# Kernel optimization log

Hardware: AMD Instinct MI355X
Metric: run time of the kernel (lower is better)

## Reference

```python
import jax, jax.numpy as jnp
import numpy as np

H = 12          # nheads
SIM_EPS = 1e-8  # SimMatrix eps
LN_EPS = 1e-5   # nn.LayerNorm default eps
SLOPE = 0.01    # LeakyReLU default negative slope


def leaky(x):
    return jnp.where(x >= 0, x, SLOPE * x)


def etc_attention(hiddens, gamma, beta, Wout, bout):
    # hiddens: [B, L, 3*D]
    B, L, D3 = hiddens.shape
    D = D3 // 3
    d = D // H
    h = hiddens.reshape(B, L, 3, H, d)
    Q = h[:, :, 0].transpose(0, 2, 1, 3)  # [B,H,L,d]
    K = h[:, :, 1].transpose(0, 2, 1, 3)
    V = h[:, :, 2].transpose(0, 2, 1, 3)
    # cosine-similarity attention scores (SimMatrix(K, Q))
    Kn = K / jnp.clip(jnp.linalg.norm(K, axis=-1, keepdims=True), SIM_EPS, None)
    Qn = Q / jnp.clip(jnp.linalg.norm(Q, axis=-1, keepdims=True), SIM_EPS, None)
    att = jnp.einsum('bhid,bhjd->bhij', Kn, Qn)  # [B,H,L,L]
    # LayerNorm over the head axis H (lnormalize: [B, L*L, H] layernorm on last dim)
    mu = att.mean(axis=1, keepdims=True)
    var = att.var(axis=1, keepdims=True)  # biased, matches torch LayerNorm
    att = (att - mu) / jnp.sqrt(var + LN_EPS)
    att = att * gamma[None, :, None, None] + beta[None, :, None, None]
    att = jax.nn.softmax(att, axis=-1)
    att = jnp.where(jnp.isnan(att), jnp.zeros_like(att), att)  # removeNaN
    out = jnp.einsum('bhij,bhjd->bhid', att, V)          # att @ V
    out = out.transpose(0, 2, 1, 3).reshape(B, L, D)      # catHiddens
    # dropout is identity at inference; lin_out = Linear + Softmax
    probs = jax.nn.softmax(out @ Wout.T + bout, axis=-1)  # [B,L,C]
    return probs, att


def get_weights(att, masks):
    # att: [B,H,L,L], masks: [B,L] float
    w = masks * att.mean(axis=1).sum(axis=1)  # [B,L]
    return jax.nn.softmax(w, axis=-1)[..., None]  # [B,L,1]


def setup_inputs() -> dict:
    key = jax.random.key(0)
    ks = jax.random.split(key, 16)
    B, L = 16, 512
    Din, D, C, VOCAB = 300, 768, 20, 32000

    def kaiming(k, shape, fan_in):
        return jax.random.normal(k, shape, jnp.float32) * np.sqrt(2.0 / fan_in)

    return {
        'input_ids': jax.random.randint(ks[0], (B, L), 0, VOCAB),
        'wv': jax.random.normal(ks[1], (B, L, Din), jnp.float32),
        'emb': jax.random.normal(ks[2], (VOCAB, D), jnp.float32),
        'W_t': kaiming(ks[3], (3 * D, D), D),
        'b_t': jnp.zeros((3 * D,), jnp.float32),
        'gamma_t': jnp.ones((H,), jnp.float32),
        'beta_t': jnp.zeros((H,), jnp.float32),
        'Wout_t': kaiming(ks[4], (C, D), D),
        'bout_t': jnp.zeros((C,), jnp.float32),
        'W_h': kaiming(ks[5], (3 * D, Din), Din),
        'b_h': jnp.zeros((3 * D,), jnp.float32),
        'gamma_h': jnp.ones((H,), jnp.float32),
        'beta_h': jnp.zeros((H,), jnp.float32),
        'Wout_h': kaiming(ks[6], (C, D), D),
        'bout_h': jnp.zeros((C,), jnp.float32),
    }


def reference(input_ids, wv, emb, W_t, b_t, gamma_t, beta_t, Wout_t, bout_t,
              W_h, b_h, gamma_h, beta_h, Wout_h, bout_h):
    masks = (input_ids != 0).astype(jnp.float32)  # [B,L]
    # token branch: Embedding -> LeakyReLU -> Linear -> LeakyReLU
    h_t = leaky(leaky(emb[input_ids]) @ W_t.T + b_t)
    probs_t, att_t = etc_attention(h_t, gamma_t, beta_t, Wout_t, bout_t)
    probs_t = (get_weights(att_t, masks) * probs_t).sum(axis=1)  # [B,C]
    # hidden/word-vector branch: Linear -> LeakyReLU
    h_h = leaky(wv @ W_h.T + b_h)
    probs_h, att_h = etc_attention(h_h, gamma_h, beta_h, Wout_h, bout_h)
    probs_h = (get_weights(att_h, masks) * probs_h).sum(axis=1)
    return (probs_t + probs_h) / 2.0
```

## Files before the change

### kernel.cpp

```cpp
#include <hip/hip_runtime.h>

typedef unsigned int uint;
typedef unsigned short ushort;
typedef _Float16 f16;
typedef _Float16 h8 __attribute__((ext_vector_type(8)));
typedef float f32x4 __attribute__((ext_vector_type(4)));


__device__ __forceinline__ float b2f(ushort u){ return __uint_as_float(((uint)u)<<16); }
__device__ __forceinline__ ushort f2b(float f){
  uint u = __float_as_uint(f);
  uint r = u + 0x7fffu + ((u>>16)&1u);
  return (ushort)(r>>16);
}
__device__ __forceinline__ float leaky(float x){ return x >= 0.f ? x : 0.01f*x; }
__device__ __forceinline__ float ldf(const void* p, int idx, int isb){
  return isb ? b2f(((const ushort*)p)[idx]) : ((const float*)p)[idx];
}

#define GLOAD16(gp, lp) __builtin_amdgcn_global_load_lds( \
    (const __attribute__((address_space(1))) void*)(gp), \
    (__attribute__((address_space(3))) void*)(lp), 16, 0, 0)

__global__ void k_detect(const ushort* __restrict__ wvbits, int* __restrict__ flag){
  if (blockIdx.x==0 && threadIdx.x==0){
    int sane = 0;
    for (int i=0;i<128;i++){
      uint e = (wvbits[i]>>7)&0xffu;
      if (e==0u || (e>=90u && e<=150u)) sane++;
    }
    *flag = (sane >= 115) ? 1 : 0;
  }
}

__global__ __launch_bounds__(256) void k_zero(float* __restrict__ colsum,
    float* __restrict__ lsum){
  int bid = blockIdx.x, tid = threadIdx.x;
  if (bid < 32) colsum[bid*256 + tid] = 0.f;
  else          lsum[(bid-32)*256 + tid] = 0.f;
}

__global__ __launch_bounds__(256) void k_build_x(const int* __restrict__ ids,
    const void* __restrict__ emb, f16* __restrict__ Ah, const int* __restrict__ flag){
  int isb = *flag;
  int t = blockIdx.x*256 + threadIdx.x;
  int m = t / 96;
  int kk = (t % 96) * 8;
  float o[8];
  if (isb){
    const ushort* src = (const ushort*)emb + (size_t)ids[m]*768 + kk;
    uint4 v = *(const uint4*)src;
    o[0]=__uint_as_float((v.x&0xffffu)<<16); o[1]=__uint_as_float(v.x&0xffff0000u);
    o[2]=__uint_as_float((v.y&0xffffu)<<16); o[3]=__uint_as_float(v.y&0xffff0000u);
    o[4]=__uint_as_float((v.z&0xffffu)<<16); o[5]=__uint_as_float(v.z&0xffff0000u);
    o[6]=__uint_as_float((v.w&0xffffu)<<16); o[7]=__uint_as_float(v.w&0xffff0000u);
  } else {
    const float* src = (const float*)emb + (size_t)ids[m]*768 + kk;
    float4 v0 = ((const float4*)src)[0];
    float4 v1 = ((const float4*)src)[1];
    o[0]=v0.x; o[1]=v0.y; o[2]=v0.z; o[3]=v0.w;
    o[4]=v1.x; o[5]=v1.y; o[6]=v1.z; o[7]=v1.w;
  }
  h8 hv;
  #pragma unroll
  for (int i=0;i<8;i++) hv[i] = (f16)leaky(o[i]);
  *(h8*)(Ah + (size_t)m*768 + kk) = hv;
}

__global__ __launch_bounds__(256) void k_prep(const void* __restrict__ src,
    f16* __restrict__ dst, int Ksrc, int kp8, const int* __restrict__ flag){
  int isb = *flag;
  int t = blockIdx.x*256 + threadIdx.x;
  int n = t / kp8;
  int kk = (t % kp8) * 8;
  h8 hv;
  #pragma unroll
  for (int i=0;i<8;i++){
    int k = kk + i;
    hv[i] = (k < Ksrc) ? (f16)ldf(src, n*Ksrc + k, isb) : (f16)0.f;
  }
  *(h8*)(dst + (size_t)n*(kp8*8) + kk) = hv;
}

template<int KP>
__global__ __launch_bounds__(256) void k_gemm_mfma(const f16* __restrict__ Ah,
    const f16* __restrict__ Wh, const void* __restrict__ bias, const int* __restrict__ flag,
    f16* __restrict__ Qh, f16* __restrict__ Kh, f16* __restrict__ Vt){
  constexpr int STEPS = KP/64;
  __shared__ __align__(16) f16 As[128*64];
  __shared__ __align__(16) f16 Bs[128*64];
  int tid = threadIdx.x;
  int w = tid >> 6, lane = tid & 63;
  int mrow = lane & 15, kq = lane >> 4;
  int m0 = blockIdx.x * 128;
  int n0 = blockIdx.y * 128;
  int msub = (w & 1) * 64, nsub = (w >> 1) * 64;

  f32x4 acc[4][4];
  #pragma unroll
  for (int mt=0; mt<4; mt++)
    #pragma unroll
    for (int nt=0; nt<4; nt++) acc[mt][nt] = (f32x4){0.f,0.f,0.f,0.f};

  int cbase = w*64 + lane;

  for (int step=0; step<STEPS; step++){
    int k0 = step*64;
    __syncthreads();
    #pragma unroll
    for (int rep=0; rep<4; rep++){
      int cb = rep*256 + w*64;
      int c  = rep*256 + cbase;
      int row = c >> 3;
      int qs  = (c & 7) ^ (row & 7);
      GLOAD16(Ah + (size_t)(m0+row)*KP + k0 + qs*8, As + cb*8);
      GLOAD16(Wh + (size_t)(n0+row)*KP + k0 + qs*8, Bs + cb*8);
    }
    __syncthreads();
    #pragma unroll
    for (int ks=0; ks<2; ks++){
      h8 af[4], bf[4];
      #pragma unroll
      for (int mt=0; mt<4; mt++){
        int row = msub + mt*16 + mrow;
        int slot = (ks*4 + kq) ^ (row & 7);
        af[mt] = *(const h8*)(As + row*64 + slot*8);
      }
      #pragma unroll
      for (int nt=0; nt<4; nt++){
        int row = nsub + nt*16 + mrow;
        int slot = (ks*4 + kq) ^ (row & 7);
        bf[nt] = *(const h8*)(Bs + row*64 + slot*8);
      }
      #pragma unroll
      for (int mt=0; mt<4; mt++)
        #pragma unroll
        for (int nt=0; nt<4; nt++)
          acc[mt][nt] = __builtin_amdgcn_mfma_f32_16x16x32_f16(af[mt], bf[nt], acc[mt][nt], 0, 0, 0);
    }
  }

  int isb = *flag;
  int n0w = n0 + nsub;
  int s = n0w / 768;
  int h = (n0w % 768) >> 6;
  float bv[4];
  #pragma unroll
  for (int nt=0; nt<4; nt++) bv[nt] = ldf(bias, n0w + nt*16 + mrow, isb);

  #pragma unroll
  for (int mt=0; mt<4; mt++){
    float yv[4][4];
    #pragma unroll
    for (int nt=0; nt<4; nt++)
      #pragma unroll
      for (int r=0; r<4; r++)
        yv[nt][r] = leaky(acc[mt][nt][r] + bv[nt]);
    if (s < 2){
      #pragma unroll
      for (int r=0; r<4; r++){
        float ss = yv[0][r]*yv[0][r] + yv[1][r]*yv[1][r]
                 + yv[2][r]*yv[2][r] + yv[3][r]*yv[3][r];
        ss += __shfl_xor(ss, 1); ss += __shfl_xor(ss, 2);
        ss += __shfl_xor(ss, 4); ss += __shfl_xor(ss, 8);
        float rn = 1.f / fmaxf(sqrtf(ss), 1e-8f);
        #pragma unroll
        for (int nt=0; nt<4; nt++) yv[nt][r] *= rn;
      }
    }
    #pragma unroll
    for (int nt=0; nt<4; nt++){
      #pragma unroll
      for (int r=0; r<4; r++){
        int m = m0 + msub + mt*16 + kq*4 + r;
        int dd = nt*16 + mrow;
        int bq = m >> 9, l = m & 511;
        float y = yv[nt][r];
        if (s == 0)      Qh[((size_t)(bq*12 + h)*512 + l)*64 + dd] = (f16)y;
        else if (s == 1) Kh[((size_t)(bq*12 + h)*512 + l)*64 + dd] = (f16)y;
        else             Vt[((size_t)(bq*12 + h)*64 + dd)*512 + l] = (f16)y;
      }
    }
  }
}

__global__ __launch_bounds__(256) void k_scores(const f16* __restrict__ Qh,
    const f16* __restrict__ Kh, const void* __restrict__ gamma,
    const void* __restrict__ beta, const int* __restrict__ flag,
    f16* __restrict__ E, float* __restrict__ lsum){
  constexpr int TS = 72;
  __shared__ f16 S[12*16*TS];
  __shared__ float gL[12], beL[12];

  int tid = threadIdx.x;
  int w = tid >> 6, lane = tid & 63;
  int kq = lane >> 4, mrow = lane & 15;
  int bx = blockIdx.x;
  int jt = bx & 7, it = (bx >> 3) & 31, b = bx >> 8;
  int i0 = it*16, j0 = jt*64;

  if (tid < 12){ int isb = *flag; gL[tid] = ldf(gamma, tid, isb); beL[tid] = ldf(beta, tid, isb); }

  #pragma unroll
  for (int hh=0; hh<3; hh++){
    int h = w*3 + hh;
    const f16* kb = Kh + ((size_t)(b*12+h)*512 + i0 + mrow)*64;
    h8 a0 = *(const h8*)(kb + kq*8);
    h8 a1 = *(const h8*)(kb + 32 + kq*8);
    const f16* qb = Qh + ((size_t)(b*12+h)*512 + j0)*64;
    #pragma unroll
    for (int jn=0; jn<4; jn++){
      const f16* qr = qb + (size_t)(jn*16 + mrow)*64;
      h8 q0 = *(const h8*)(qr + kq*8);
      h8 q1 = *(const h8*)(qr + 32 + kq*8);
      f32x4 c = (f32x4){0.f,0.f,0.f,0.f};
      c = __builtin_amdgcn_mfma_f32_16x16x32_f16(a0, q0, c, 0, 0, 0);
      c = __builtin_amdgcn_mfma_f32_16x16x32_f16(a1, q1, c, 0, 0, 0);
      #pragma unroll
      for (int r=0;r<4;r++)
        S[(h*16 + kq*4 + r)*TS + jn*16 + mrow] = (f16)c[r];
    }
  }
  __syncthreads();
  int pj = tid & 63, piw = tid >> 6;
  #pragma unroll
  for (int p=0; p<4; p++){
    int i = piw*4 + p;
    float s[12];
    float mu = 0.f, sq = 0.f;
    #pragma unroll
    for (int h=0;h<12;h++){ s[h] = (float)S[(h*16+i)*TS + pj]; mu += s[h]; sq += s[h]*s[h]; }
    mu *= (1.f/12.f);
    float var = fmaxf(sq*(1.f/12.f) - mu*mu, 0.f);
    float rstd = rsqrtf(var + 1e-5f);
    #pragma unroll
    for (int h=0;h<12;h++){
      float e = __expf((s[h]-mu)*rstd*gL[h] + beL[h]);
      S[(h*16+i)*TS + pj] = (f16)e;
    }
  }
  __syncthreads();
  if (tid < 192){
    int h = tid >> 4, i = tid & 15;
    const f16* zr = &S[(h*16 + i)*TS];
    float ssum = 0.f;
    #pragma unroll
    for (int q=0;q<8;q++){
      h8 v = *(const h8*)(zr + q*8);
      #pragma unroll
      for (int t=0;t<8;t++) ssum += (float)v[t];
    }
    atomicAdd(&lsum[(size_t)(b*12+h)*512 + i0 + i], ssum);
  }
  #pragma unroll
  for (int u0=0; u0<6; u0++){
    int u = tid + u0*256;
    int h = u >> 7, rem = u & 127, i = rem >> 3, q = rem & 7;
    h8 v = *(const h8*)&S[(h*16 + i)*TS + q*8];
    *(h8*)(E + ((size_t)(b*12+h)*512 + i0 + i)*512 + j0 + q*8) = v;
  }
}

__global__ __launch_bounds__(256) void k_pv2(const f16* __restrict__ E,
    const f16* __restrict__ Vt, const float* __restrict__ lsum,
    float* __restrict__ O, float* __restrict__ colsum){
  __shared__ float csL[512];
  int tid = threadIdx.x;
  int w = tid >> 6, lane = tid & 63;
  int kq = lane >> 4, mrow = lane & 15;
  int b = blockIdx.y;
  int h = blockIdx.x >> 3, it = blockIdx.x & 7;
  int i0w = it*64 + w*16;

  csL[tid] = 0.f; csL[tid + 256] = 0.f;
  float rinv = 1.f / lsum[(size_t)(b*12+h)*512 + i0w + mrow];
  __syncthreads();

  const f16* erow  = E  + ((size_t)(b*12+h)*512 + i0w + mrow)*512 + kq*8;
  const f16* vbase = Vt + ((size_t)(b*12+h)*64 + mrow)*512 + kq*8;

  f32x4 acc[4];
  #pragma unroll
  for (int nt=0; nt<4; nt++) acc[nt] = (f32x4){0.f,0.f,0.f,0.f};

  #pragma unroll 4
  for (int jt=0; jt<16; jt++){
    int j0 = jt*32;
    h8 ea  = *(const h8*)(erow + j0);
    h8 bf0 = *(const h8*)(vbase + j0);
    h8 bf1 = *(const h8*)(vbase + (size_t)16*512 + j0);
    h8 bf2 = *(const h8*)(vbase + (size_t)32*512 + j0);
    h8 bf3 = *(const h8*)(vbase + (size_t)48*512 + j0);
    acc[0] = __builtin_amdgcn_mfma_f32_16x16x32_f16(ea, bf0, acc[0], 0, 0, 0);
    acc[1] = __builtin_amdgcn_mfma_f32_16x16x32_f16(ea, bf1, acc[1], 0, 0, 0);
    acc[2] = __builtin_amdgcn_mfma_f32_16x16x32_f16(ea, bf2, acc[2], 0, 0, 0);
    acc[3] = __builtin_amdgcn_mfma_f32_16x16x32_f16(ea, bf3, acc[3], 0, 0, 0);
    float cs[8];
    #pragma unroll
    for (int t=0;t<8;t++) cs[t] = (float)ea[t] * rinv;
    #pragma unroll
    for (int t=0;t<8;t++){
      cs[t] += __shfl_xor(cs[t], 1); cs[t] += __shfl_xor(cs[t], 2);
      cs[t] += __shfl_xor(cs[t], 4); cs[t] += __shfl_xor(cs[t], 8);
    }
    if (mrow == 0){
      #pragma unroll
      for (int t=0;t<8;t++) atomicAdd(&csL[j0 + kq*8 + t], cs[t]);
    }
  }
  __syncthreads();
  atomicAdd(&colsum[b*512 + tid],       csL[tid]       * (1.f/12.f));
  atomicAdd(&colsum[b*512 + 256 + tid], csL[tid + 256] * (1.f/12.f));

  #pragma unroll
  for (int r=0; r<4; r++){
    float g = __shfl(rinv, kq*4 + r);
    #pragma unroll
    for (int nt=0; nt<4; nt++)
      O[((size_t)(b*512) + i0w + kq*4 + r)*768 + h*64 + nt*16 + mrow] = acc[nt][r] * g;
  }
}

__global__ __launch_bounds__(256) void k_attn2(const f16* __restrict__ Qh,
    const f16* __restrict__ Kh, const f16* __restrict__ Vt,
    const void* __restrict__ gamma, const void* __restrict__ beta,
    const int* __restrict__ flag,
    float* __restrict__ O, float* __restrict__ colsum){
  constexpr int ZS = 421;
  constexpr int TS = 40;
  __shared__ float z[16*ZS];
  __shared__ f16   zt[12*16*TS];
  __shared__ float rsL[192];
  __shared__ float csL[32];
  __shared__ float gL[12], beL[12];

  int tid = threadIdx.x;
  int w = tid >> 6, lane = tid & 63;
  int kq = lane >> 4, mrow = lane & 15;
  int bx = blockIdx.x;
  int b = bx >> 5, i0 = (bx & 31) << 4;
  int pj = tid & 31, pi = tid >> 5;

  if (tid < 12){ int isb = *flag; gL[tid] = ldf(gamma, tid, isb); beL[tid] = ldf(beta, tid, isb); }
  if (tid < 32) csL[tid] = 0.f;

  h8 ak[3][2];
  #pragma unroll
  for (int hh=0; hh<3; hh++){
    int h = w*3 + hh;
    const f16* kb = Kh + ((size_t)(b*12+h)*512 + i0 + mrow)*64;
    #pragma unroll
    for (int ks=0; ks<2; ks++)
      ak[hh][ks] = *(const h8*)(kb + ks*32 + kq*8);
  }
  f32x4 oacc[3][4];
  #pragma unroll
  for (int hh=0; hh<3; hh++)
    #pragma unroll
    for (int nt=0; nt<4; nt++)
      oacc[hh][nt] = (f32x4){0.f,0.f,0.f,0.f};
  float racc[2][12];
  #pragma unroll
  for (int p=0;p<2;p++)
    #pragma unroll
    for (int h=0;h<12;h++) racc[p][h] = 0.f;

  __syncthreads();

  for (int sweep=0; sweep<2; sweep++){
    for (int jt=0; jt<16; jt++){
      #pragma unroll
      for (int hh=0; hh<3; hh++){
        int h = w*3 + hh;
        const f16* qb = Qh + ((size_t)(b*12+h)*512 + jt*32)*64;
        #pragma unroll
        for (int jn=0; jn<2; jn++){
          f32x4 c = (f32x4){0.f,0.f,0.f,0.f};
          #pragma unroll
          for (int ks=0; ks<2; ks++){
            h8 bf = *(const h8*)(qb + (size_t)(jn*16 + mrow)*64 + ks*32 + kq*8);
            c = __builtin_amdgcn_mfma_f32_16x16x32_f16(ak[hh][ks], bf, c, 0, 0, 0);
          }
          int jl = jn*16 + mrow;
          #pragma unroll
          for (int r=0;r<4;r++)
            z[(kq*4 + r)*ZS + jl*13 + h] = c[r];
        }
      }
      __syncthreads();
      #pragma unroll
      for (int p=0; p<2; p++){
        int i = pi + p*8, j = pj;
        const float* zp = &z[i*ZS + j*13];
        float s[12];
        float mu = 0.f, sq = 0.f;
        #pragma unroll
        for (int h=0;h<12;h++){ s[h] = zp[h]; mu += s[h]; sq += s[h]*s[h]; }
        mu *= (1.f/12.f);
        float var = fmaxf(sq*(1.f/12.f) - mu*mu, 0.f);
        float rstd = rsqrtf(var + 1e-5f);
        if (sweep == 0){
          #pragma unroll
          for (int h=0;h<12;h++){
            float e = __expf((s[h]-mu)*rstd*gL[h] + beL[h]);
            racc[p][h] += e;
          }
        } else {
          float cacc = 0.f;
          #pragma unroll
          for (int h=0;h<12;h++){
            float e = __expf((s[h]-mu)*rstd*gL[h] + beL[h]);
            zt[(h*16 + i)*TS + j] = (f16)e;
            cacc += e * rsL[h*16 + i];
          }
          atomicAdd(&csL[j], cacc*(1.f/12.f));
        }
      }
      if (sweep == 0){
        __syncthreads();
      } else {
        __syncthreads();
        #pragma unroll
        for (int hh=0; hh<3; hh++){
          int h = w*3 + hh;
          h8 pa = *(const h8*)&zt[(h*16 + mrow)*TS + kq*8];
          const f16* vb = Vt + ((size_t)(b*12+h)*64)*512;
          #pragma unroll
          for (int nt=0; nt<4; nt++){
            h8 bf = *(const h8*)(vb + (size_t)(nt*16 + mrow)*512 + jt*32 + kq*8);
            oacc[hh][nt] = __builtin_amdgcn_mfma_f32_16x16x32_f16(pa, bf, oacc[hh][nt], 0, 0, 0);
          }
        }
        if (tid < 32){
          atomicAdd(&colsum[b*512 + jt*32 + tid], csL[tid]);
          csL[tid] = 0.f;
        }
      }
    }
    if (sweep == 0){
      #pragma unroll
      for (int p=0;p<2;p++){
        #pragma unroll
        for (int h=0;h<12;h++){
          float v = racc[p][h];
          #pragma unroll
          for (int m=1; m<32; m<<=1) v += __shfl_xor(v, m);
          if ((lane & 31) == 0) rsL[h*16 + (pi + p*8)] = 1.f / v;
        }
      }
      __syncthreads();
    }
  }
  #pragma unroll
  for (int hh=0; hh<3; hh++){
    int h = w*3 + hh;
    #pragma unroll
    for (int nt=0; nt<4; nt++){
      #pragma unroll
      for (int r=0;r<4;r++){
        int i = kq*4 + r;
        float val = oacc[hh][nt][r] * rsL[h*16 + i];
        O[((size_t)(b*512) + i0 + i)*768 + h*64 + nt*16 + mrow] = val;
      }
    }
  }
}

__global__ __launch_bounds__(256) void k_probs(const float* __restrict__ O,
    const void* __restrict__ Wout, const void* __restrict__ bout,
    const int* __restrict__ flag, float* __restrict__ probs){
  int isb = *flag;
  int tid = threadIdx.x, wv = tid>>6, lane = tid&63;
  int m = blockIdx.x*4 + wv;
  const float* orow = O + (size_t)m*768;
  float acc[20];
  #pragma unroll
  for (int c=0;c<20;c++) acc[c]=0.f;
  for (int kk=0; kk<12; kk++){
    float o = orow[kk*64 + lane];
    #pragma unroll
    for (int c=0;c<20;c++)
      acc[c] += o * ldf(Wout, c*768 + kk*64 + lane, isb);
  }
  #pragma unroll
  for (int c=0;c<20;c++){
    #pragma unroll
    for (int off=1; off<64; off<<=1) acc[c] += __shfl_xor(acc[c], off, 64);
  }
  float mx = -3.4e38f;
  #pragma unroll
  for (int c=0;c<20;c++){ acc[c] += ldf(bout, c, isb); mx = fmaxf(mx, acc[c]); }
  float s=0.f;
  #pragma unroll
  for (int c=0;c<20;c++){ acc[c] = __expf(acc[c]-mx); s += acc[c]; }
  float inv = 1.f/s;
  if (lane == 0){
    float* pr = probs + (size_t)m*20;
    #pragma unroll
    for (int c=0;c<20;c++) pr[c] = acc[c]*inv;
  }
}

__global__ __launch_bounds__(512) void k_final(const int* __restrict__ ids,
    const float* __restrict__ colsum, const float* __restrict__ probs,
    const int* __restrict__ flag,
    float* __restrict__ accb, void* __restrict__ outp, int br){
  __shared__ float red[8];
  __shared__ float bcast;
  __shared__ float pacc[8][20];
  int b = blockIdx.x, tid = threadIdx.x;
  int wv = tid>>6, lane = tid&63;
  float w = (ids[b*512+tid] != 0) ? colsum[b*512+tid] : 0.f;
  float mx = w;
  #pragma unroll
  for (int off=1; off<64; off<<=1) mx = fmaxf(mx, __shfl_xor(mx, off, 64));
  if (lane==0) red[wv] = mx;
  __syncthreads();
  if (tid==0){ float m2 = red[0]; for (int k2=1;k2<8;k2++) m2 = fmaxf(m2, red[k2]); bcast = m2; }
  __syncthreads();
  float M = bcast;
  float e = __expf(w - M);
  float s = e;
  #pragma unroll
  for (int off=1; off<64; off<<=1) s += __shfl_xor(s, off, 64);
  if (lane==0) red[wv] = s;
  __syncthreads();
  if (tid==0){ float s2=0.f; for (int k2=0;k2<8;k2++) s2 += red[k2]; bcast = s2; }
  __syncthreads();
  float wn = e / bcast;
  float p[20];
  const float* pr = probs + ((size_t)b*512 + tid)*20;
  #pragma unroll
  for (int c=0;c<20;c++) p[c] = wn * pr[c];
  #pragma unroll
  for (int c=0;c<20;c++){
    #pragma unroll
    for (int off=1; off<64; off<<=1) p[c] += __shfl_xor(p[c], off, 64);
  }
  if (lane==0){
    #pragma unroll
    for (int c=0;c<20;c++) pacc[wv][c] = p[c];
  }
  __syncthreads();
  if (tid < 20){
    float s2 = 0.f;
    #pragma unroll
    for (int k2=0;k2<8;k2++) s2 += pacc[k2][tid];
    if (br == 0) accb[b*20 + tid] = s2;
    else {
      float v = (accb[b*20 + tid] + s2) * 0.5f;
      if (*flag) ((ushort*)outp)[b*20 + tid] = f2b(v);
      else       ((float*)outp)[b*20 + tid] = v;
    }
  }
}

extern "C" void kernel_launch(void* const* d_in, const int* in_sizes, int n_in,
                              void* d_out, int out_size, void* d_ws, size_t ws_size,
                              hipStream_t stream){
  (void)in_sizes; (void)n_in; (void)out_size;
  const int*  ids = (const int*)d_in[0];
  const void* wvp = d_in[1];
  const void* emb = d_in[2];
  const void* Wt[2]  = {d_in[3], d_in[9]};
  const void* bt[2]  = {d_in[4], d_in[10]};
  const void* gm[2]  = {d_in[5], d_in[11]};
  const void* bet[2] = {d_in[6], d_in[12]};
  const void* Wo[2]  = {d_in[7], d_in[13]};
  const void* bo[2]  = {d_in[8], d_in[14]};

  float*  O      = (float*)d_ws;
  f16*    Qh     = (f16*)(O + 6291456);
  f16*    Kh     = Qh + 6291456;
  f16*    Vt     = Kh + 6291456;
  f16*    Ah     = Vt + 6291456;
  f16*    Wh     = Ah + 6291456;
  float*  probsb = (float*)(Wh + 1769472);
  float*  colsum = probsb + 163840;
  float*  accb   = colsum + 8192;
  int*    flagp  = (int*)(accb + 320);
  float*  lsum   = (float*)(flagp + 4);
  f16*    E      = (f16*)(lsum + 98304);
  size_t  need   = (size_t)((char*)(E + 50331648) - (char*)d_ws);
  int bigws = (ws_size >= need);

  k_detect<<<1, 64, 0, stream>>>((const ushort*)wvp, flagp);

  for (int br=0; br<2; br++){
    if (br==0){
      k_build_x<<<3072, 256, 0, stream>>>(ids, emb, Ah, flagp);
      k_prep<<<864, 256, 0, stream>>>(Wt[0], Wh, 768, 96, flagp);
    } else {
      k_prep<<<1280, 256, 0, stream>>>(wvp, Ah, 300, 40, flagp);
      k_prep<<<360, 256, 0, stream>>>(Wt[1], Wh, 300, 40, flagp);
    }
    k_zero<<<416, 256, 0, stream>>>(colsum, lsum);
    dim3 g1(64, 18);
    if (br==0) k_gemm_mfma<768><<<g1, 256, 0, stream>>>(Ah, Wh, bt[0], flagp, Qh, Kh, Vt);
    else       k_gemm_mfma<320><<<g1, 256, 0, stream>>>(Ah, Wh, bt[1], flagp, Qh, Kh, Vt);
    if (bigws){
      k_scores<<<4096, 256, 0, stream>>>(Qh, Kh, gm[br], bet[br], flagp, E, lsum);
      dim3 gpv(96, 16);
      k_pv2<<<gpv, 256, 0, stream>>>(E, Vt, lsum, O, colsum);
    } else {
      k_attn2<<<512, 256, 0, stream>>>(Qh, Kh, Vt, gm[br], bet[br], flagp, O, colsum);
    }
    k_probs<<<2048, 256, 0, stream>>>(O, Wo[br], bo[br], flagp, probsb);
    k_final<<<16, 512, 0, stream>>>(ids, colsum, probsb, flagp, accb, d_out, br);
  }
}
```

Before: 622.3 us.

## Batch both branches into merged prep, GEMM, probs and final launches

Merges the flag-detect and zeroing kernels into one init kernel, and fuses all input/weight conversion into a single prep kernel. The QKV GEMM for both branches now runs in one launch via a z-dimension, as do the output projections, and a single final kernel combines both branches. This removes about ten kernel launches and lets the two branches' small kernels fill the GPU together. In exchange it needs separate workspace buffers per branch, and the fallback path now always uses the large-E scores path while the old small-workspace fused attention kernel is dropped.

```diff
diff --git a/kernel.cpp b/kernel.cpp
--- a/kernel.cpp
+++ b/kernel.cpp
@@ -22,73 +22,102 @@
     (const __attribute__((address_space(1))) void*)(gp), \
     (__attribute__((address_space(3))) void*)(lp), 16, 0, 0)
 
-__global__ void k_detect(const ushort* __restrict__ wvbits, int* __restrict__ flag){
-  if (blockIdx.x==0 && threadIdx.x==0){
-    int sane = 0;
-    for (int i=0;i<128;i++){
-      uint e = (wvbits[i]>>7)&0xffu;
-      if (e==0u || (e>=90u && e<=150u)) sane++;
-    }
-    *flag = (sane >= 115) ? 1 : 0;
-  }
-}
-
-__global__ __launch_bounds__(256) void k_zero(float* __restrict__ colsum,
-    float* __restrict__ lsum){
+__global__ __launch_bounds__(256) void k_init(const ushort* __restrict__ wvbits,
+    int* __restrict__ flag, float* __restrict__ zbase){
   int bid = blockIdx.x, tid = threadIdx.x;
-  if (bid < 32) colsum[bid*256 + tid] = 0.f;
-  else          lsum[(bid-32)*256 + tid] = 0.f;
-}
-
-__global__ __launch_bounds__(256) void k_build_x(const int* __restrict__ ids,
-    const void* __restrict__ emb, f16* __restrict__ Ah, const int* __restrict__ flag){
+  if (bid == 0){
+    if (tid == 0){
+      int sane = 0;
+      for (int i=0;i<128;i++){
+        uint e = (wvbits[i]>>7)&0xffu;
+        if (e==0u || (e>=90u && e<=150u)) sane++;
+      }
+      *flag = (sane >= 115) ? 1 : 0;
+    }
+  } else {
+    zbase[(bid-1)*256 + tid] = 0.f;
+  }
+}
+
+__global__ __launch_bounds__(256) void k_prep_all(const int* __restrict__ ids,
+    const void* __restrict__ emb, const void* __restrict__ wv,
+    const void* __restrict__ W0, const void* __restrict__ W1,
+    const int* __restrict__ flag,
+    f16* __restrict__ AhA, f16* __restrict__ WhA,
+    f16* __restrict__ AhB, f16* __restrict__ WhB,
+    int nBX, int nW0, int nA1, int nW1){
   int isb = *flag;
-  int t = blockIdx.x*256 + threadIdx.x;
-  int m = t / 96;
-  int kk = (t % 96) * 8;
-  float o[8];
-  if (isb){
-    const ushort* src = (const ushort*)emb + (size_t)ids[m]*768 + kk;
-    uint4 v = *(const uint4*)src;
-    o[0]=__uint_as_float((v.x&0xffffu)<<16); o[1]=__uint_as_float(v.x&0xffff0000u);
-    o[2]=__uint_as_float((v.y&0xffffu)<<16); o[3]=__uint_as_float(v.y&0xffff0000u);
-    o[4]=__uint_as_float((v.z&0xffffu)<<16); o[5]=__uint_as_float(v.z&0xffff0000u);
-    o[6]=__uint_as_float((v.w&0xffffu)<<16); o[7]=__uint_as_float(v.w&0xffff0000u);
+  int bx = blockIdx.x, tid = threadIdx.x;
+  if (bx < nBX){
+    int t = bx*256 + tid;
+    int m = t / 96, kk = (t % 96) * 8;
+    float o[8];
+    if (isb){
+      const ushort* src = (const ushort*)emb + (size_t)ids[m]*768 + kk;
+      uint4 v = *(const uint4*)src;
+      o[0]=__uint_as_float((v.x&0xffffu)<<16); o[1]=__uint_as_float(v.x&0xffff0000u);
+      o[2]=__uint_as_float((v.y&0xffffu)<<16); o[3]=__uint_as_float(v.y&0xffff0000u);
+      o[4]=__uint_as_float((v.z&0xffffu)<<16); o[5]=__uint_as_float(v.z&0xffff0000u);
+      o[6]=__uint_as_float((v.w&0xffffu)<<16); o[7]=__uint_as_float(v.w&0xffff0000u);
+    } else {
+      const float* src = (const float*)emb + (size_t)ids[m]*768 + kk;
+      float4 v0 = ((const float4*)src)[0];
+      float4 v1 = ((const float4*)src)[1];
+      o[0]=v0.x; o[1]=v0.y; o[2]=v0.z; o[3]=v0.w;
+      o[4]=v1.x; o[5]=v1.y; o[6]=v1.z; o[7]=v1.w;
+    }
+    h8 hv;
+    #pragma unroll
+    for (int i=0;i<8;i++) hv[i] = (f16)leaky(o[i]);
+    *(h8*)(AhA + (size_t)m*768 + kk) = hv;
+  } else if (bx < nBX + nW0){
+    int t = (bx - nBX)*256 + tid;
+    int n = t / 96, kk = (t % 96) * 8;
+    h8 hv;
+    #pragma unroll
+    for (int i=0;i<8;i++) hv[i] = (f16)ldf(W0, n*768 + kk + i, isb);
+    *(h8*)(WhA + (size_t)n*768 + kk) = hv;
+  } else if (bx < nBX + nW0 + nA1){
+    int t = (bx - nBX - nW0)*256 + tid;
+    int n = t / 40, kk = (t % 40) * 8;
+    h8 hv;
+    #pragma unroll
+    for (int i=0;i<8;i++){
+      int k = kk + i;
+      hv[i] = (k < 300) ? (f16)ldf(wv, n*300 + k, isb) : (f16)0.f;
+    }
+    *(h8*)(AhB + (size_t)n*320 + kk) = hv;
   } else {
-    const float* src = (const float*)emb + (size_t)ids[m]*768 + kk;
-    float4 v0 = ((const float4*)src)[0];
-    float4 v1 = ((const float4*)src)[1];
-    o[0]=v0.x; o[1]=v0.y; o[2]=v0.z; o[3]=v0.w;
-    o[4]=v1.x; o[5]=v1.y; o[6]=v1.z; o[7]=v1.w;
-  }
-  h8 hv;
-  #pragma unroll
-  for (int i=0;i<8;i++) hv[i] = (f16)leaky(o[i]);
-  *(h8*)(Ah + (size_t)m*768 + kk) = hv;
-}
-
-__global__ __launch_bounds__(256) void k_prep(const void* __restrict__ src,
-    f16* __restrict__ dst, int Ksrc, int kp8, const int* __restrict__ flag){
-  int isb = *flag;
-  int t = blockIdx.x*256 + threadIdx.x;
-  int n = t / kp8;
-  int kk = (t % kp8) * 8;
-  h8 hv;
-  #pragma unroll
-  for (int i=0;i<8;i++){
-    int k = kk + i;
-    hv[i] = (k < Ksrc) ? (f16)ldf(src, n*Ksrc + k, isb) : (f16)0.f;
-  }
-  *(h8*)(dst + (size_t)n*(kp8*8) + kk) = hv;
-}
-
-template<int KP>
-__global__ __launch_bounds__(256) void k_gemm_mfma(const f16* __restrict__ Ah,
-    const f16* __restrict__ Wh, const void* __restrict__ bias, const int* __restrict__ flag,
-    f16* __restrict__ Qh, f16* __restrict__ Kh, f16* __restrict__ Vt){
-  constexpr int STEPS = KP/64;
+    int t = (bx - nBX - nW0 - nA1)*256 + tid;
+    int n = t / 40, kk = (t % 40) * 8;
+    h8 hv;
+    #pragma unroll
+    for (int i=0;i<8;i++){
+      int k = kk + i;
+      hv[i] = (k < 300) ? (f16)ldf(W1, n*300 + k, isb) : (f16)0.f;
+    }
+    *(h8*)(WhB + (size_t)n*320 + kk) = hv;
+  }
+}
+
+__global__ __launch_bounds__(256) void k_gemm_m(
+    const f16* AhA, const f16* WhA, const void* biasA, int KA,
+    f16* QhA, f16* KhA, f16* VtA,
+    const f16* AhB, const f16* WhB, const void* biasB, int KB,
+    f16* QhB, f16* KhB, f16* VtB,
+    const int* __restrict__ flag, int sbase){
   __shared__ __align__(16) f16 As[128*64];
   __shared__ __align__(16) f16 Bs[128*64];
+  int z = sbase + blockIdx.z;
+  const f16* Ah = z ? AhB : AhA;
+  const f16* Wh = z ? WhB : WhA;
+  const void* bias = z ? biasB : biasA;
+  int KP = z ? KB : KA;
+  f16* Qh = z ? QhB : QhA;
+  f16* Kh = z ? KhB : KhA;
+  f16* Vt = z ? VtB : VtA;
+  int STEPS = KP >> 6;
+
   int tid = threadIdx.x;
   int w = tid >> 6, lane = tid & 63;
   int mrow = lane & 15, kq = lane >> 4;
@@ -321,154 +350,14 @@
   }
 }
 
-__global__ __launch_bounds__(256) void k_attn2(const f16* __restrict__ Qh,
-    const f16* __restrict__ Kh, const f16* __restrict__ Vt,
-    const void* __restrict__ gamma, const void* __restrict__ beta,
-    const int* __restrict__ flag,
-    float* __restrict__ O, float* __restrict__ colsum){
-  constexpr int ZS = 421;
-  constexpr int TS = 40;
-  __shared__ float z[16*ZS];
-  __shared__ f16   zt[12*16*TS];
-  __shared__ float rsL[192];
-  __shared__ float csL[32];
-  __shared__ float gL[12], beL[12];
-
-  int tid = threadIdx.x;
-  int w = tid >> 6, lane = tid & 63;
-  int kq = lane >> 4, mrow = lane & 15;
-  int bx = blockIdx.x;
-  int b = bx >> 5, i0 = (bx & 31) << 4;
-  int pj = tid & 31, pi = tid >> 5;
-
-  if (tid < 12){ int isb = *flag; gL[tid] = ldf(gamma, tid, isb); beL[tid] = ldf(beta, tid, isb); }
-  if (tid < 32) csL[tid] = 0.f;
-
-  h8 ak[3][2];
-  #pragma unroll
-  for (int hh=0; hh<3; hh++){
-    int h = w*3 + hh;
-    const f16* kb = Kh + ((size_t)(b*12+h)*512 + i0 + mrow)*64;
-    #pragma unroll
-    for (int ks=0; ks<2; ks++)
-      ak[hh][ks] = *(const h8*)(kb + ks*32 + kq*8);
-  }
-  f32x4 oacc[3][4];
-  #pragma unroll
-  for (int hh=0; hh<3; hh++)
-    #pragma unroll
-    for (int nt=0; nt<4; nt++)
-      oacc[hh][nt] = (f32x4){0.f,0.f,0.f,0.f};
-  float racc[2][12];
-  #pragma unroll
-  for (int p=0;p<2;p++)
-    #pragma unroll
-    for (int h=0;h<12;h++) racc[p][h] = 0.f;
-
-  __syncthreads();
-
-  for (int sweep=0; sweep<2; sweep++){
-    for (int jt=0; jt<16; jt++){
-      #pragma unroll
-      for (int hh=0; hh<3; hh++){
-        int h = w*3 + hh;
-        const f16* qb = Qh + ((size_t)(b*12+h)*512 + jt*32)*64;
-        #pragma unroll
-        for (int jn=0; jn<2; jn++){
-          f32x4 c = (f32x4){0.f,0.f,0.f,0.f};
-          #pragma unroll
-          for (int ks=0; ks<2; ks++){
-            h8 bf = *(const h8*)(qb + (size_t)(jn*16 + mrow)*64 + ks*32 + kq*8);
-            c = __builtin_amdgcn_mfma_f32_16x16x32_f16(ak[hh][ks], bf, c, 0, 0, 0);
-          }
-          int jl = jn*16 + mrow;
-          #pragma unroll
-          for (int r=0;r<4;r++)
-            z[(kq*4 + r)*ZS + jl*13 + h] = c[r];
-        }
-      }
-      __syncthreads();
-      #pragma unroll
-      for (int p=0; p<2; p++){
-        int i = pi + p*8, j = pj;
-        const float* zp = &z[i*ZS + j*13];
-        float s[12];
-        float mu = 0.f, sq = 0.f;
-        #pragma unroll
-        for (int h=0;h<12;h++){ s[h] = zp[h]; mu += s[h]; sq += s[h]*s[h]; }
-        mu *= (1.f/12.f);
-        float var = fmaxf(sq*(1.f/12.f) - mu*mu, 0.f);
-        float rstd = rsqrtf(var + 1e-5f);
-        if (sweep == 0){
-          #pragma unroll
-          for (int h=0;h<12;h++){
-            float e = __expf((s[h]-mu)*rstd*gL[h] + beL[h]);
-            racc[p][h] += e;
-          }
-        } else {
-          float cacc = 0.f;
-          #pragma unroll
-          for (int h=0;h<12;h++){
-            float e = __expf((s[h]-mu)*rstd*gL[h] + beL[h]);
-            zt[(h*16 + i)*TS + j] = (f16)e;
-            cacc += e * rsL[h*16 + i];
-          }
-          atomicAdd(&csL[j], cacc*(1.f/12.f));
-        }
-      }
-      if (sweep == 0){
-        __syncthreads();
-      } else {
-        __syncthreads();
-        #pragma unroll
-        for (int hh=0; hh<3; hh++){
-          int h = w*3 + hh;
-          h8 pa = *(const h8*)&zt[(h*16 + mrow)*TS + kq*8];
-          const f16* vb = Vt + ((size_t)(b*12+h)*64)*512;
-          #pragma unroll
-          for (int nt=0; nt<4; nt++){
-            h8 bf = *(const h8*)(vb + (size_t)(nt*16 + mrow)*512 + jt*32 + kq*8);
-            oacc[hh][nt] = __builtin_amdgcn_mfma_f32_16x16x32_f16(pa, bf, oacc[hh][nt], 0, 0, 0);
-          }
-        }
-        if (tid < 32){
-          atomicAdd(&colsum[b*512 + jt*32 + tid], csL[tid]);
-          csL[tid] = 0.f;
-        }
-      }
-    }
-    if (sweep == 0){
-      #pragma unroll
-      for (int p=0;p<2;p++){
-        #pragma unroll
-        for (int h=0;h<12;h++){
-          float v = racc[p][h];
-          #pragma unroll
-          for (int m=1; m<32; m<<=1) v += __shfl_xor(v, m);
-          if ((lane & 31) == 0) rsL[h*16 + (pi + p*8)] = 1.f / v;
-        }
-      }
-      __syncthreads();
-    }
-  }
-  #pragma unroll
-  for (int hh=0; hh<3; hh++){
-    int h = w*3 + hh;
-    #pragma unroll
-    for (int nt=0; nt<4; nt++){
-      #pragma unroll
-      for (int r=0;r<4;r++){
-        int i = kq*4 + r;
-        float val = oacc[hh][nt][r] * rsL[h*16 + i];
-        O[((size_t)(b*512) + i0 + i)*768 + h*64 + nt*16 + mrow] = val;
-      }
-    }
-  }
-}
-
-__global__ __launch_bounds__(256) void k_probs(const float* __restrict__ O,
-    const void* __restrict__ Wout, const void* __restrict__ bout,
-    const int* __restrict__ flag, float* __restrict__ probs){
+__global__ __launch_bounds__(256) void k_probs_m(const float* OA, const float* OB,
+    const void* WoA, const void* WoB, const void* boA, const void* boB,
+    float* prA, float* prB, const int* __restrict__ flag, int sbase){
+  int z = sbase + blockIdx.y;
+  const float* O = z ? OB : OA;
+  const void* Wout = z ? WoB : WoA;
+  const void* bout = z ? boB : boA;
+  float* probs = z ? prB : prA;
   int isb = *flag;
   int tid = threadIdx.x, wv = tid>>6, lane = tid&63;
   int m = blockIdx.x*4 + wv;
@@ -501,57 +390,65 @@
   }
 }
 
-__global__ __launch_bounds__(512) void k_final(const int* __restrict__ ids,
-    const float* __restrict__ colsum, const float* __restrict__ probs,
-    const int* __restrict__ flag,
-    float* __restrict__ accb, void* __restrict__ outp, int br){
+__global__ __launch_bounds__(512) void k_final_m(const int* __restrict__ ids,
+    const float* __restrict__ cs0, const float* __restrict__ cs1,
+    const float* __restrict__ pr0, const float* __restrict__ pr1,
+    const int* __restrict__ flag, void* __restrict__ outp){
   __shared__ float red[8];
   __shared__ float bcast;
   __shared__ float pacc[8][20];
+  __shared__ float osum[20];
   int b = blockIdx.x, tid = threadIdx.x;
   int wv = tid>>6, lane = tid&63;
-  float w = (ids[b*512+tid] != 0) ? colsum[b*512+tid] : 0.f;
-  float mx = w;
-  #pragma unroll
-  for (int off=1; off<64; off<<=1) mx = fmaxf(mx, __shfl_xor(mx, off, 64));
-  if (lane==0) red[wv] = mx;
-  __syncthreads();
-  if (tid==0){ float m2 = red[0]; for (int k2=1;k2<8;k2++) m2 = fmaxf(m2, red[k2]); bcast = m2; }
-  __syncthreads();
-  float M = bcast;
-  float e = __expf(w - M);
-  float s = e;
-  #pragma unroll
-  for (int off=1; off<64; off<<=1) s += __shfl_xor(s, off, 64);
-  if (lane==0) red[wv] = s;
-  __syncthreads();
-  if (tid==0){ float s2=0.f; for (int k2=0;k2<8;k2++) s2 += red[k2]; bcast = s2; }
-  __syncthreads();
-  float wn = e / bcast;
-  float p[20];
-  const float* pr = probs + ((size_t)b*512 + tid)*20;
-  #pragma unroll
-  for (int c=0;c<20;c++) p[c] = wn * pr[c];
-  #pragma unroll
-  for (int c=0;c<20;c++){
-    #pragma unroll
-    for (int off=1; off<64; off<<=1) p[c] += __shfl_xor(p[c], off, 64);
-  }
-  if (lane==0){
-    #pragma unroll
-    for (int c=0;c<20;c++) pacc[wv][c] = p[c];
-  }
-  __syncthreads();
+  int msk = (ids[b*512+tid] != 0);
+  for (int br=0; br<2; br++){
+    const float* colsum = br ? cs1 : cs0;
+    const float* probs  = br ? pr1 : pr0;
+    float w = msk ? colsum[b*512+tid] : 0.f;
+    float mx = w;
+    #pragma unroll
+    for (int off=1; off<64; off<<=1) mx = fmaxf(mx, __shfl_xor(mx, off, 64));
+    if (lane==0) red[wv] = mx;
+    __syncthreads();
+    if (tid==0){ float m2 = red[0]; for (int k2=1;k2<8;k2++) m2 = fmaxf(m2, red[k2]); bcast = m2; }
+    __syncthreads();
+    float M = bcast;
+    float e = __expf(w - M);
+    float s = e;
+    #pragma unroll
+    for (int off=1; off<64; off<<=1) s += __shfl_xor(s, off, 64);
+    if (lane==0) red[wv] = s;
+    __syncthreads();
+    if (tid==0){ float s2=0.f; for (int k2=0;k2<8;k2++) s2 += red[k2]; bcast = s2; }
+    __syncthreads();
+    float wn = e / bcast;
+    float p[20];
+    const float* pr = probs + ((size_t)b*512 + tid)*20;
+    #pragma unroll
+    for (int c=0;c<20;c++) p[c] = wn * pr[c];
+    #pragma unroll
+    for (int c=0;c<20;c++){
+      #pragma unroll
+      for (int off=1; off<64; off<<=1) p[c] += __shfl_xor(p[c], off, 64);
+    }
+    if (lane==0){
+      #pragma unroll
+      for (int c=0;c<20;c++) pacc[wv][c] = p[c];
+    }
+    __syncthreads();
+    if (tid < 20){
+      float s2 = 0.f;
+      #pragma unroll
+      for (int k2=0;k2<8;k2++) s2 += pacc[k2][tid];
+      if (br == 0) osum[tid] = s2;
+      else         osum[tid] += s2;
+    }
+    __syncthreads();
+  }
   if (tid < 20){
-    float s2 = 0.f;
-    #pragma unroll
-    for (int k2=0;k2<8;k2++) s2 += pacc[k2][tid];
-    if (br == 0) accb[b*20 + tid] = s2;
-    else {
-      float v = (accb[b*20 + tid] + s2) * 0.5f;
-      if (*flag) ((ushort*)outp)[b*20 + tid] = f2b(v);
-      else       ((float*)outp)[b*20 + tid] = v;
-    }
+    float v = osum[tid] * 0.5f;
+    if (*flag) ((ushort*)outp)[b*20 + tid] = f2b(v);
+    else       ((float*)outp)[b*20 + tid] = v;
   }
 }
 
@@ -569,43 +466,76 @@
   const void* Wo[2]  = {d_in[7], d_in[13]};
   const void* bo[2]  = {d_in[8], d_in[14]};
 
-  float*  O      = (float*)d_ws;
-  f16*    Qh     = (f16*)(O + 6291456);
-  f16*    Kh     = Qh + 6291456;
-  f16*    Vt     = Kh + 6291456;
-  f16*    Ah     = Vt + 6291456;
-  f16*    Wh     = Ah + 6291456;
-  float*  probsb = (float*)(Wh + 1769472);
-  float*  colsum = probsb + 163840;
-  float*  accb   = colsum + 8192;
-  int*    flagp  = (int*)(accb + 320);
-  float*  lsum   = (float*)(flagp + 4);
-  f16*    E      = (f16*)(lsum + 98304);
-  size_t  need   = (size_t)((char*)(E + 50331648) - (char*)d_ws);
-  int bigws = (ws_size >= need);
-
-  k_detect<<<1, 64, 0, stream>>>((const ushort*)wvp, flagp);
-
-  for (int br=0; br<2; br++){
-    if (br==0){
-      k_build_x<<<3072, 256, 0, stream>>>(ids, emb, Ah, flagp);
-      k_prep<<<864, 256, 0, stream>>>(Wt[0], Wh, 768, 96, flagp);
-    } else {
-      k_prep<<<1280, 256, 0, stream>>>(wvp, Ah, 300, 40, flagp);
-      k_prep<<<360, 256, 0, stream>>>(Wt[1], Wh, 300, 40, flagp);
-    }
-    k_zero<<<416, 256, 0, stream>>>(colsum, lsum);
-    dim3 g1(64, 18);
-    if (br==0) k_gemm_mfma<768><<<g1, 256, 0, stream>>>(Ah, Wh, bt[0], flagp, Qh, Kh, Vt);
-    else       k_gemm_mfma<320><<<g1, 256, 0, stream>>>(Ah, Wh, bt[1], flagp, Qh, Kh, Vt);
-    if (bigws){
-      k_scores<<<4096, 256, 0, stream>>>(Qh, Kh, gm[br], bet[br], flagp, E, lsum);
-      dim3 gpv(96, 16);
-      k_pv2<<<gpv, 256, 0, stream>>>(E, Vt, lsum, O, colsum);
-    } else {
-      k_attn2<<<512, 256, 0, stream>>>(Qh, Kh, Vt, gm[br], bet[br], flagp, O, colsum);
-    }
-    k_probs<<<2048, 256, 0, stream>>>(O, Wo[br], bo[br], flagp, probsb);
-    k_final<<<16, 512, 0, stream>>>(ids, colsum, probsb, flagp, accb, d_out, br);
-  }
-}
+  char* p = (char*)d_ws;
+  #define ALLOC(ty, name, cnt) ty* name = (ty*)p; p += sizeof(ty)*(size_t)(cnt)
+
+  p = (char*)d_ws;
+  ALLOC(float, O0, 6291456);
+  ALLOC(float, O1, 6291456);
+  ALLOC(f16, Qh0, 6291456); ALLOC(f16, Kh0, 6291456); ALLOC(f16, Vt0, 6291456);
+  ALLOC(f16, Qh1, 6291456); ALLOC(f16, Kh1, 6291456); ALLOC(f16, Vt1, 6291456);
+  ALLOC(f16, Ah0, 6291456); ALLOC(f16, Wh0, 1769472);
+  ALLOC(f16, Ah1, 2621440); ALLOC(f16, Wh1, 737280);
+  ALLOC(float, probs0, 163840); ALLOC(float, probs1, 163840);
+  ALLOC(float, zb_big, 212992);
+  ALLOC(int, flag_big, 4);
+  ALLOC(f16, E_big, 50331648);
+  size_t needBig = (size_t)(p - (char*)d_ws);
+
+  if (ws_size >= needBig){
+    float* colsum0 = zb_big;          float* colsum1 = zb_big + 8192;
+    float* lsum0   = zb_big + 16384;  float* lsum1   = zb_big + 16384 + 98304;
+    int* flagp = flag_big; f16* E = E_big;
+
+    k_init<<<833, 256, 0, stream>>>((const ushort*)wvp, flagp, zb_big);
+    k_prep_all<<<3072+864+1280+360, 256, 0, stream>>>(ids, emb, wvp, Wt[0], Wt[1],
+        flagp, Ah0, Wh0, Ah1, Wh1, 3072, 864, 1280, 360);
+    dim3 gg(64, 18, 2);
+    k_gemm_m<<<gg, 256, 0, stream>>>(Ah0, Wh0, bt[0], 768, Qh0, Kh0, Vt0,
+                                     Ah1, Wh1, bt[1], 320, Qh1, Kh1, Vt1, flagp, 0);
+    dim3 gpv(96, 16);
+    k_scores<<<4096, 256, 0, stream>>>(Qh0, Kh0, gm[0], bet[0], flagp, E, lsum0);
+    k_pv2<<<gpv, 256, 0, stream>>>(E, Vt0, lsum0, O0, colsum0);
+    k_scores<<<4096, 256, 0, stream>>>(Qh1, Kh1, gm[1], bet[1], flagp, E, lsum1);
+    k_pv2<<<gpv, 256, 0, stream>>>(E, Vt1, lsum1, O1, colsum1);
+    dim3 gpr(2048, 2);
+    k_probs_m<<<gpr, 256, 0, stream>>>(O0, O1, Wo[0], Wo[1], bo[0], bo[1],
+                                       probs0, probs1, flagp, 0);
+    k_final_m<<<16, 512, 0, stream>>>(ids, colsum0, colsum1, probs0, probs1, flagp, d_out);
+    return;
+  }
+
+  p = (char*)d_ws;
+  ALLOC(float, O, 6291456);
+  ALLOC(f16, Qh, 6291456); ALLOC(f16, Kh, 6291456); ALLOC(f16, Vt, 6291456);
+  ALLOC(f16, Ah, 6291456); ALLOC(f16, Wh, 1769472);
+  ALLOC(float, probsA, 163840); ALLOC(float, probsB, 163840);
+  ALLOC(float, zb, 212992);
+  ALLOC(int, flagm, 4);
+  ALLOC(f16, Em, 50331648);
+  float* colsum0 = zb;          float* colsum1 = zb + 8192;
+  float* lsum0   = zb + 16384;  float* lsum1   = zb + 16384 + 98304;
+
+  k_init<<<833, 256, 0, stream>>>((const ushort*)wvp, flagm, zb);
+  k_prep_all<<<3072+864, 256, 0, stream>>>(ids, emb, wvp, Wt[0], Wt[1],
+      flagm, Ah, Wh, Ah, Wh, 3072, 864, 0, 0);
+  dim3 g1(64, 18, 1);
+  k_gemm_m<<<g1, 256, 0, stream>>>(Ah, Wh, bt[0], 768, Qh, Kh, Vt,
+                                   Ah, Wh, bt[0], 768, Qh, Kh, Vt, flagm, 0);
+  dim3 gpv(96, 16);
+  k_scores<<<4096, 256, 0, stream>>>(Qh, Kh, gm[0], bet[0], flagm, Em, lsum0);
+  k_pv2<<<gpv, 256, 0, stream>>>(Em, Vt, lsum0, O, colsum0);
+  dim3 gpr(2048, 1);
+  k_probs_m<<<gpr, 256, 0, stream>>>(O, O, Wo[0], Wo[1], bo[0], bo[1],
+                                     probsA, probsB, flagm, 0);
+  k_prep_all<<<1280+360, 256, 0, stream>>>(ids, emb, wvp, Wt[0], Wt[1],
+      flagm, Ah, Wh, Ah, Wh, 0, 0, 1280, 360);
+  k_gemm_m<<<g1, 256, 0, stream>>>(Ah, Wh, bt[1], 320, Qh, Kh, Vt,
+                                   Ah, Wh, bt[1], 320, Qh, Kh, Vt, flagm, 0);
+  k_scores<<<4096, 256, 0, stream>>>(Qh, Kh, gm[1], bet[1], flagm, Em, lsum1);
+  k_pv2<<<gpv, 256, 0, stream>>>(Em, Vt, lsum1, O, colsum1);
+  k_probs_m<<<gpr, 256, 0, stream>>>(O, O, Wo[0], Wo[1], bo[0], bo[1],
+                                     probsA, probsB, flagm, 1);
+  k_final_m<<<16, 512, 0, stream>>>(ids, colsum0, colsum1, probsA, probsB, flagm, d_out);
+  #undef ALLOC
+}
```

Result: faster. 577.9 us (-7.1%).
